# Kernel tuning notes

Measured on AMD Instinct MI355X. Metric: run time of the kernel, lower is better.

The kernel has to match this reference:

```python
import jax, jax.numpy as jnp
import numpy as np

N, D, L = 8192, 256, 3
DEGREE_P = 0.0078  # ~64 avg degree


def _normalize_adj(g):
    # symmetric normalization with self-loops: D^-1/2 (A + I) D^-1/2
    n = g.shape[0]
    a = g + jnp.eye(n, dtype=g.dtype)
    deg = jnp.sum(a, axis=1)
    dinv = jnp.where(deg > 0, jax.lax.rsqrt(deg), 0.0)
    return a * dinv[:, None] * dinv[None, :]


def _gcn(gn, h, W, b):
    # GCN layer (eval mode, dropout p=0): aggregate -> linear -> relu
    h = gn @ h                      # [N, D] adjacency aggregation
    return jax.nn.relu(h @ W.T + b)  # [N, D]


def setup_inputs() -> dict:
    key = jax.random.key(0)
    ks = jax.random.split(key, 8)
    # sparse binary symmetric adjacency stored dense
    g = (jax.random.uniform(ks[0], (N, N)) < DEGREE_P).astype(jnp.float32)
    g = jnp.maximum(g, g.T)
    h = jax.random.normal(ks[1], (N, D), dtype=jnp.float32)
    s = 1.0 / np.sqrt(D)
    W_down = jax.random.normal(ks[2], (L, D, D), dtype=jnp.float32) * s
    b_down = jnp.zeros((L, D), dtype=jnp.float32)
    W_bottom = jax.random.normal(ks[3], (D, D), dtype=jnp.float32) * s
    b_bottom = jnp.zeros((D,), dtype=jnp.float32)
    W_up = jax.random.normal(ks[4], (L, D, D), dtype=jnp.float32) * s
    b_up = jnp.zeros((L, D), dtype=jnp.float32)
    return dict(g=g, h=h, W_down=W_down, b_down=b_down,
                W_bottom=W_bottom, b_bottom=b_bottom,
                W_up=W_up, b_up=b_up)


def reference(g, h, W_down, b_down, W_bottom, b_bottom, W_up, b_up):
    gn = _normalize_adj(g)
    l_n = W_down.shape[0]
    org_h = h
    down_outs = []
    for i in range(l_n):
        h = _gcn(gn, h, W_down[i], b_down[i])
        down_outs.append(h)
    h = _gcn(gn, h, W_bottom, b_bottom)
    hs = []
    for i in range(l_n):
        h = h + down_outs[l_n - i - 1]   # skip connection
        h = _gcn(gn, h, W_up[i], b_up[i])
        hs.append(h)
    hs.append(h + org_h)
    return jnp.stack(hs)  # [l_n+1, N, D]
```

## Files before the change

### kernel.cpp

```cpp
#include <hip/hip_runtime.h>
#include <cstdint>
#include <cstddef>


#define GN 8192
#define GD 256
#define CAP 320

typedef unsigned int uint32;
using frag_ab = __attribute__((ext_vector_type(8))) short;
using frag_cd = __attribute__((ext_vector_type(4))) float;

static __device__ inline unsigned short f2bf(float x) {
    uint32 u = __float_as_uint(x);
    u += 0x7fffu + ((u >> 16) & 1u);
    return (unsigned short)(u >> 16);
}

__global__ __launch_bounds__(256) void k_build(const float* __restrict__ g,
                                               unsigned short* __restrict__ col,
                                               int* __restrict__ cnt,
                                               float* __restrict__ dinv)
{
    __shared__ int s_cnt;
    const int i = blockIdx.x;
    const int tid = threadIdx.x;
    if (tid == 0) s_cnt = 0;
    __syncthreads();
    const float4* grow = (const float4*)(g + (size_t)i * GN);
    unsigned short* crow = col + (size_t)i * CAP;
    for (int j4 = tid; j4 < GN / 4; j4 += 256) {
        float4 v = grow[j4];
        int j = j4 * 4;
        if (v.x != 0.0f) { int p = atomicAdd(&s_cnt, 1); if (p < CAP) crow[p] = (unsigned short)(j + 0); }
        if (v.y != 0.0f) { int p = atomicAdd(&s_cnt, 1); if (p < CAP) crow[p] = (unsigned short)(j + 1); }
        if (v.z != 0.0f) { int p = atomicAdd(&s_cnt, 1); if (p < CAP) crow[p] = (unsigned short)(j + 2); }
        if (v.w != 0.0f) { int p = atomicAdd(&s_cnt, 1); if (p < CAP) crow[p] = (unsigned short)(j + 3); }
    }
    __syncthreads();
    if (tid == 0) {
        int n = s_cnt; if (n > CAP) n = CAP;
        cnt[i] = n;
        dinv[i] = rsqrtf((float)s_cnt + 1.0f);
        int n8 = (n + 7) & ~7;
        for (int k = n; k < n8; ++k)
            if (k < CAP) crow[k] = (unsigned short)i;
    }
}

__global__ __launch_bounds__(256) void k_scale(const float* __restrict__ h,
                                               const float* __restrict__ dinv,
                                               unsigned short* __restrict__ hs_bf)
{
    int idx = blockIdx.x * 256 + threadIdx.x;
    float4 v = ((const float4*)h)[idx];
    int row = idx / (GD / 4);
    float dv = dinv[row];
    ushort4 r;
    r.x = f2bf(v.x * dv); r.y = f2bf(v.y * dv);
    r.z = f2bf(v.z * dv); r.w = f2bf(v.w * dv);
    ((ushort4*)hs_bf)[idx] = r;
}

__global__ __launch_bounds__(256) void k_f2bf(const float* __restrict__ src,
                                              unsigned short* __restrict__ dst)
{
    int idx = blockIdx.x * 256 + threadIdx.x;
    float4 v = ((const float4*)src)[idx];
    ushort4 r;
    r.x = f2bf(v.x); r.y = f2bf(v.y); r.z = f2bf(v.z); r.w = f2bf(v.w);
    ((ushort4*)dst)[idx] = r;
}

__global__ __launch_bounds__(256) void k_spmm(const uint32* __restrict__ hsw,
                                              const unsigned short* __restrict__ col,
                                              const int* __restrict__ cnt,
                                              const float* __restrict__ dinv,
                                              uint32* __restrict__ yw)
{
    const int tid  = threadIdx.x;
    const int lw   = tid >> 6;
    const int lane = tid & 63;
    const int i = blockIdx.x * 4 + lw;
    const int n = cnt[i];
    int n8 = (n + 7) & ~7; if (n8 > CAP) n8 = CAP;
    const uint4* idxp = (const uint4*)(col + (size_t)i * CAP);
    const uint32* lbase = hsw + lane * 2;

    float a0=0.f,a1=0.f,a2=0.f,a3=0.f;
    float b0=0.f,b1=0.f,b2=0.f,b3=0.f;

    for (int t8 = 0; t8 < n8; t8 += 8) {
        uint4 packed = idxp[t8 >> 3];
        uint32 p0 = (uint32)__builtin_amdgcn_readfirstlane((int)packed.x);
        uint32 p1 = (uint32)__builtin_amdgcn_readfirstlane((int)packed.y);
        uint32 p2 = (uint32)__builtin_amdgcn_readfirstlane((int)packed.z);
        uint32 p3 = (uint32)__builtin_amdgcn_readfirstlane((int)packed.w);
        const int c0 = (int)(p0 & 0xffffu), c1 = (int)(p0 >> 16);
        const int c2 = (int)(p1 & 0xffffu), c3 = (int)(p1 >> 16);
        const int c4 = (int)(p2 & 0xffffu), c5 = (int)(p2 >> 16);
        const int c6 = (int)(p3 & 0xffffu), c7 = (int)(p3 >> 16);
        uint2 u0 = *(const uint2*)(lbase + (size_t)c0 * 128);
        uint2 u1 = *(const uint2*)(lbase + (size_t)c1 * 128);
        uint2 u2 = *(const uint2*)(lbase + (size_t)c2 * 128);
        uint2 u3 = *(const uint2*)(lbase + (size_t)c3 * 128);
        uint2 u4 = *(const uint2*)(lbase + (size_t)c4 * 128);
        uint2 u5 = *(const uint2*)(lbase + (size_t)c5 * 128);
        uint2 u6 = *(const uint2*)(lbase + (size_t)c6 * 128);
        uint2 u7 = *(const uint2*)(lbase + (size_t)c7 * 128);
        a0 += __uint_as_float(u0.x << 16); a1 += __uint_as_float(u0.x & 0xffff0000u);
        a2 += __uint_as_float(u0.y << 16); a3 += __uint_as_float(u0.y & 0xffff0000u);
        b0 += __uint_as_float(u1.x << 16); b1 += __uint_as_float(u1.x & 0xffff0000u);
        b2 += __uint_as_float(u1.y << 16); b3 += __uint_as_float(u1.y & 0xffff0000u);
        a0 += __uint_as_float(u2.x << 16); a1 += __uint_as_float(u2.x & 0xffff0000u);
        a2 += __uint_as_float(u2.y << 16); a3 += __uint_as_float(u2.y & 0xffff0000u);
        b0 += __uint_as_float(u3.x << 16); b1 += __uint_as_float(u3.x & 0xffff0000u);
        b2 += __uint_as_float(u3.y << 16); b3 += __uint_as_float(u3.y & 0xffff0000u);
        a0 += __uint_as_float(u4.x << 16); a1 += __uint_as_float(u4.x & 0xffff0000u);
        a2 += __uint_as_float(u4.y << 16); a3 += __uint_as_float(u4.y & 0xffff0000u);
        b0 += __uint_as_float(u5.x << 16); b1 += __uint_as_float(u5.x & 0xffff0000u);
        b2 += __uint_as_float(u5.y << 16); b3 += __uint_as_float(u5.y & 0xffff0000u);
        a0 += __uint_as_float(u6.x << 16); a1 += __uint_as_float(u6.x & 0xffff0000u);
        a2 += __uint_as_float(u6.y << 16); a3 += __uint_as_float(u6.y & 0xffff0000u);
        b0 += __uint_as_float(u7.x << 16); b1 += __uint_as_float(u7.x & 0xffff0000u);
        b2 += __uint_as_float(u7.y << 16); b3 += __uint_as_float(u7.y & 0xffff0000u);
    }

    uint2 us = *(const uint2*)(lbase + (size_t)i * 128);
    const float coeff = (float)(1 - (n8 - n));
    a0 += coeff * __uint_as_float(us.x << 16);
    a1 += coeff * __uint_as_float(us.x & 0xffff0000u);
    a2 += coeff * __uint_as_float(us.y << 16);
    a3 += coeff * __uint_as_float(us.y & 0xffff0000u);

    const float dv = dinv[i];
    a0 = (a0 + b0) * dv; a1 = (a1 + b1) * dv;
    a2 = (a2 + b2) * dv; a3 = (a3 + b3) * dv;
    uint2 r;
    r.x = (uint32)f2bf(a0) | ((uint32)f2bf(a1) << 16);
    r.y = (uint32)f2bf(a2) | ((uint32)f2bf(a3) << 16);
    *(uint2*)(yw + (size_t)i * 128 + lane * 2) = r;
}

__global__ __launch_bounds__(256) void k_gemm(const unsigned short* __restrict__ Y,
                                              const unsigned short* __restrict__ W,
                                              const float* __restrict__ bias,
                                              const float* __restrict__ dinv,
                                              const float* __restrict__ skip,
                                              float* __restrict__ h_out,
                                              unsigned short* __restrict__ hs_out,
                                              float* __restrict__ sum_out,
                                              const float* __restrict__ add_src)
{
    const int tid  = threadIdx.x;
    const int w    = tid >> 6;
    const int lane = tid & 63;
    const int quad = lane >> 4;
    const int l16  = lane & 15;
    const int m0 = blockIdx.x * 64 + w * 16;
    const int n0 = blockIdx.y * 64;

    frag_cd acc0 = {0.f,0.f,0.f,0.f}, acc1 = {0.f,0.f,0.f,0.f};
    frag_cd acc2 = {0.f,0.f,0.f,0.f}, acc3 = {0.f,0.f,0.f,0.f};

    const size_t abase  = (size_t)(m0 + l16) * GD + quad * 8;
    const size_t bbase0 = (size_t)(n0 +  0 + l16) * GD + quad * 8;
    const size_t bbase1 = (size_t)(n0 + 16 + l16) * GD + quad * 8;
    const size_t bbase2 = (size_t)(n0 + 32 + l16) * GD + quad * 8;
    const size_t bbase3 = (size_t)(n0 + 48 + l16) * GD + quad * 8;

#pragma unroll
    for (int k0 = 0; k0 < GD; k0 += 32) {
        frag_ab a  = *(const frag_ab*)(Y + abase  + k0);
        frag_ab b0 = *(const frag_ab*)(W + bbase0 + k0);
        frag_ab b1 = *(const frag_ab*)(W + bbase1 + k0);
        frag_ab b2 = *(const frag_ab*)(W + bbase2 + k0);
        frag_ab b3 = *(const frag_ab*)(W + bbase3 + k0);
        acc0 = __builtin_amdgcn_mfma_f32_16x16x32_bf16(a, b0, acc0, 0, 0, 0);
        acc1 = __builtin_amdgcn_mfma_f32_16x16x32_bf16(a, b1, acc1, 0, 0, 0);
        acc2 = __builtin_amdgcn_mfma_f32_16x16x32_bf16(a, b2, acc2, 0, 0, 0);
        acc3 = __builtin_amdgcn_mfma_f32_16x16x32_bf16(a, b3, acc3, 0, 0, 0);
    }

    const float bn0 = bias[n0 +  0 + l16];
    const float bn1 = bias[n0 + 16 + l16];
    const float bn2 = bias[n0 + 32 + l16];
    const float bn3 = bias[n0 + 48 + l16];

#pragma unroll
    for (int reg = 0; reg < 4; ++reg) {
        const int m = m0 + quad * 4 + reg;
        const float dv = dinv[m];
        float v[4];
        v[0] = fmaxf(acc0[reg] + bn0, 0.f);
        v[1] = fmaxf(acc1[reg] + bn1, 0.f);
        v[2] = fmaxf(acc2[reg] + bn2, 0.f);
        v[3] = fmaxf(acc3[reg] + bn3, 0.f);
#pragma unroll
        for (int nt = 0; nt < 4; ++nt) {
            const size_t idx = (size_t)m * GD + n0 + nt * 16 + l16;
            const float x = v[nt];
            if (h_out)  h_out[idx] = x;
            if (hs_out) {
                float s = skip ? skip[idx] : 0.f;
                hs_out[idx] = f2bf(dv * (x + s));
            }
            if (sum_out) sum_out[idx] = x + add_src[idx];
        }
    }
}

extern "C" void kernel_launch(void* const* d_in, const int* in_sizes, int n_in,
                              void* d_out, int out_size, void* d_ws, size_t ws_size,
                              hipStream_t stream)
{
    const float* g  = (const float*)d_in[0];
    const float* h  = (const float*)d_in[1];
    const float* Wd = (const float*)d_in[2];
    const float* bd = (const float*)d_in[3];
    const float* Wb = (const float*)d_in[4];
    const float* bb = (const float*)d_in[5];
    const float* Wu = (const float*)d_in[6];
    const float* bu = (const float*)d_in[7];
    float* out = (float*)d_out;

    char* ws = (char*)d_ws;
    float*          dinv = (float*)ws;
    int*            cnt  = (int*)(ws + 32 * 1024);
    unsigned short* col  = (unsigned short*)(ws + 64 * 1024);
    size_t off = 64 * 1024 + (size_t)GN * CAP * sizeof(unsigned short);
    off = (off + 255) & ~(size_t)255;
    unsigned short* hs_bf = (unsigned short*)(ws + off); off += (size_t)GN * GD * 2;
    unsigned short* y_bf  = (unsigned short*)(ws + off); off += (size_t)GN * GD * 2;
    unsigned short* w_bf  = (unsigned short*)(ws + off); off += (size_t)7 * GD * GD * 2;
    off = (off + 255) & ~(size_t)255;
    float* dbuf1 = (float*)(ws + off); off += (size_t)GN * GD * 4;
    float* dbuf2 = (float*)(ws + off); off += (size_t)GN * GD * 4;
    float* dbuf3 = (float*)(ws + off); off += (size_t)GN * GD * 4;
    (void)ws_size; (void)in_sizes; (void)n_in; (void)out_size;

    const size_t ND = (size_t)GN * GD;
    const int WSZ = GD * GD;
    dim3 ggrid(GN / 64, GD / 64);
    dim3 sgrid(GN / 4);

    k_build<<<GN, 256, 0, stream>>>(g, col, cnt, dinv);
    k_scale<<<GN * GD / 4 / 256, 256, 0, stream>>>(h, dinv, hs_bf);
    k_f2bf<<<3 * WSZ / 4 / 256, 256, 0, stream>>>(Wd, w_bf + 0 * (size_t)WSZ);
    k_f2bf<<<1 * WSZ / 4 / 256, 256, 0, stream>>>(Wb, w_bf + 3 * (size_t)WSZ);
    k_f2bf<<<3 * WSZ / 4 / 256, 256, 0, stream>>>(Wu, w_bf + 4 * (size_t)WSZ);

    k_spmm<<<sgrid, 256, 0, stream>>>((const uint32*)hs_bf, col, cnt, dinv, (uint32*)y_bf);
    k_gemm<<<ggrid, 256, 0, stream>>>(y_bf, w_bf + 0 * (size_t)WSZ, bd + 0 * GD, dinv, nullptr, dbuf1, hs_bf, nullptr, nullptr);
    k_spmm<<<sgrid, 256, 0, stream>>>((const uint32*)hs_bf, col, cnt, dinv, (uint32*)y_bf);
    k_gemm<<<ggrid, 256, 0, stream>>>(y_bf, w_bf + 1 * (size_t)WSZ, bd + 1 * GD, dinv, nullptr, dbuf2, hs_bf, nullptr, nullptr);
    k_spmm<<<sgrid, 256, 0, stream>>>((const uint32*)hs_bf, col, cnt, dinv, (uint32*)y_bf);
    k_gemm<<<ggrid, 256, 0, stream>>>(y_bf, w_bf + 2 * (size_t)WSZ, bd + 2 * GD, dinv, nullptr, dbuf3, hs_bf, nullptr, nullptr);

    k_spmm<<<sgrid, 256, 0, stream>>>((const uint32*)hs_bf, col, cnt, dinv, (uint32*)y_bf);
    k_gemm<<<ggrid, 256, 0, stream>>>(y_bf, w_bf + 3 * (size_t)WSZ, bb, dinv, dbuf3, nullptr, hs_bf, nullptr, nullptr);

    k_spmm<<<sgrid, 256, 0, stream>>>((const uint32*)hs_bf, col, cnt, dinv, (uint32*)y_bf);
    k_gemm<<<ggrid, 256, 0, stream>>>(y_bf, w_bf + 4 * (size_t)WSZ, bu + 0 * GD, dinv, dbuf2, out + 0 * ND, hs_bf, nullptr, nullptr);
    k_spmm<<<sgrid, 256, 0, stream>>>((const uint32*)hs_bf, col, cnt, dinv, (uint32*)y_bf);
    k_gemm<<<ggrid, 256, 0, stream>>>(y_bf, w_bf + 5 * (size_t)WSZ, bu + 1 * GD, dinv, dbuf1, out + 1 * ND, hs_bf, nullptr, nullptr);
    k_spmm<<<sgrid, 256, 0, stream>>>((const uint32*)hs_bf, col, cnt, dinv, (uint32*)y_bf);
    k_gemm<<<ggrid, 256, 0, stream>>>(y_bf, w_bf + 6 * (size_t)WSZ, bu + 2 * GD, dinv, nullptr, out + 2 * ND, nullptr, out + 3 * ND, h);
}
```

Measured before the change: 785.3 us.

## Fuse SpMM aggregation and GEMM into one per-layer kernel with LDS staging

```diff
diff --git a/kernel.cpp b/kernel.cpp
--- a/kernel.cpp
+++ b/kernel.cpp
@@ -15,6 +15,9 @@
     uint32 u = __float_as_uint(x);
     u += 0x7fffu + ((u >> 16) & 1u);
     return (unsigned short)(u >> 16);
+}
+static __device__ inline uint32 pack2bf(float lo, float hi) {
+    return (uint32)f2bf(lo) | ((uint32)f2bf(hi) << 16);
 }
 
 __global__ __launch_bounds__(256) void k_build(const float* __restrict__ g,
@@ -42,9 +45,6 @@
         int n = s_cnt; if (n > CAP) n = CAP;
         cnt[i] = n;
         dinv[i] = rsqrtf((float)s_cnt + 1.0f);
-        int n8 = (n + 7) & ~7;
-        for (int k = n; k < n8; ++k)
-            if (k < CAP) crow[k] = (unsigned short)i;
     }
 }
 
@@ -72,98 +72,89 @@
     ((ushort4*)dst)[idx] = r;
 }
 
-__global__ __launch_bounds__(256) void k_spmm(const uint32* __restrict__ hsw,
-                                              const unsigned short* __restrict__ col,
-                                              const int* __restrict__ cnt,
-                                              const float* __restrict__ dinv,
-                                              uint32* __restrict__ yw)
-{
-    const int tid  = threadIdx.x;
-    const int lw   = tid >> 6;
-    const int lane = tid & 63;
-    const int i = blockIdx.x * 4 + lw;
-    const int n = cnt[i];
-    int n8 = (n + 7) & ~7; if (n8 > CAP) n8 = CAP;
-    const uint4* idxp = (const uint4*)(col + (size_t)i * CAP);
-    const uint32* lbase = hsw + lane * 2;
-
-    float a0=0.f,a1=0.f,a2=0.f,a3=0.f;
-    float b0=0.f,b1=0.f,b2=0.f,b3=0.f;
-
-    for (int t8 = 0; t8 < n8; t8 += 8) {
-        uint4 packed = idxp[t8 >> 3];
-        uint32 p0 = (uint32)__builtin_amdgcn_readfirstlane((int)packed.x);
-        uint32 p1 = (uint32)__builtin_amdgcn_readfirstlane((int)packed.y);
-        uint32 p2 = (uint32)__builtin_amdgcn_readfirstlane((int)packed.z);
-        uint32 p3 = (uint32)__builtin_amdgcn_readfirstlane((int)packed.w);
-        const int c0 = (int)(p0 & 0xffffu), c1 = (int)(p0 >> 16);
-        const int c2 = (int)(p1 & 0xffffu), c3 = (int)(p1 >> 16);
-        const int c4 = (int)(p2 & 0xffffu), c5 = (int)(p2 >> 16);
-        const int c6 = (int)(p3 & 0xffffu), c7 = (int)(p3 >> 16);
-        uint2 u0 = *(const uint2*)(lbase + (size_t)c0 * 128);
-        uint2 u1 = *(const uint2*)(lbase + (size_t)c1 * 128);
-        uint2 u2 = *(const uint2*)(lbase + (size_t)c2 * 128);
-        uint2 u3 = *(const uint2*)(lbase + (size_t)c3 * 128);
-        uint2 u4 = *(const uint2*)(lbase + (size_t)c4 * 128);
-        uint2 u5 = *(const uint2*)(lbase + (size_t)c5 * 128);
-        uint2 u6 = *(const uint2*)(lbase + (size_t)c6 * 128);
-        uint2 u7 = *(const uint2*)(lbase + (size_t)c7 * 128);
-        a0 += __uint_as_float(u0.x << 16); a1 += __uint_as_float(u0.x & 0xffff0000u);
-        a2 += __uint_as_float(u0.y << 16); a3 += __uint_as_float(u0.y & 0xffff0000u);
-        b0 += __uint_as_float(u1.x << 16); b1 += __uint_as_float(u1.x & 0xffff0000u);
-        b2 += __uint_as_float(u1.y << 16); b3 += __uint_as_float(u1.y & 0xffff0000u);
-        a0 += __uint_as_float(u2.x << 16); a1 += __uint_as_float(u2.x & 0xffff0000u);
-        a2 += __uint_as_float(u2.y << 16); a3 += __uint_as_float(u2.y & 0xffff0000u);
-        b0 += __uint_as_float(u3.x << 16); b1 += __uint_as_float(u3.x & 0xffff0000u);
-        b2 += __uint_as_float(u3.y << 16); b3 += __uint_as_float(u3.y & 0xffff0000u);
-        a0 += __uint_as_float(u4.x << 16); a1 += __uint_as_float(u4.x & 0xffff0000u);
-        a2 += __uint_as_float(u4.y << 16); a3 += __uint_as_float(u4.y & 0xffff0000u);
-        b0 += __uint_as_float(u5.x << 16); b1 += __uint_as_float(u5.x & 0xffff0000u);
-        b2 += __uint_as_float(u5.y << 16); b3 += __uint_as_float(u5.y & 0xffff0000u);
-        a0 += __uint_as_float(u6.x << 16); a1 += __uint_as_float(u6.x & 0xffff0000u);
-        a2 += __uint_as_float(u6.y << 16); a3 += __uint_as_float(u6.y & 0xffff0000u);
-        b0 += __uint_as_float(u7.x << 16); b1 += __uint_as_float(u7.x & 0xffff0000u);
-        b2 += __uint_as_float(u7.y << 16); b3 += __uint_as_float(u7.y & 0xffff0000u);
-    }
-
-    uint2 us = *(const uint2*)(lbase + (size_t)i * 128);
-    const float coeff = (float)(1 - (n8 - n));
-    a0 += coeff * __uint_as_float(us.x << 16);
-    a1 += coeff * __uint_as_float(us.x & 0xffff0000u);
-    a2 += coeff * __uint_as_float(us.y << 16);
-    a3 += coeff * __uint_as_float(us.y & 0xffff0000u);
-
-    const float dv = dinv[i];
-    a0 = (a0 + b0) * dv; a1 = (a1 + b1) * dv;
-    a2 = (a2 + b2) * dv; a3 = (a3 + b3) * dv;
-    uint2 r;
-    r.x = (uint32)f2bf(a0) | ((uint32)f2bf(a1) << 16);
-    r.y = (uint32)f2bf(a2) | ((uint32)f2bf(a3) << 16);
-    *(uint2*)(yw + (size_t)i * 128 + lane * 2) = r;
-}
-
-__global__ __launch_bounds__(256) void k_gemm(const unsigned short* __restrict__ Y,
-                                              const unsigned short* __restrict__ W,
-                                              const float* __restrict__ bias,
-                                              const float* __restrict__ dinv,
-                                              const float* __restrict__ skip,
-                                              float* __restrict__ h_out,
-                                              unsigned short* __restrict__ hs_out,
-                                              float* __restrict__ sum_out,
-                                              const float* __restrict__ add_src)
-{
+__global__ __launch_bounds__(256) void k_layer(const uint32* __restrict__ hs_in,
+                                               const unsigned short* __restrict__ col,
+                                               const int* __restrict__ cnt,
+                                               const float* __restrict__ dinv,
+                                               const unsigned short* __restrict__ W,
+                                               const float* __restrict__ bias,
+                                               const float* __restrict__ skip,
+                                               float* __restrict__ h_out,
+                                               unsigned short* __restrict__ hs_out,
+                                               float* __restrict__ sum_out,
+                                               const float* __restrict__ add_src)
+{
+    __shared__ unsigned short s_idx[16][CAP];
+    __shared__ unsigned short s_y[16][264];
     const int tid  = threadIdx.x;
     const int w    = tid >> 6;
     const int lane = tid & 63;
+    const int m0   = blockIdx.x * 16;
+
+    const uint32* lbase = hs_in + lane * 2;
+#pragma unroll 1
+    for (int rr = 0; rr < 4; ++rr) {
+        const int lrow = w * 4 + rr;
+        const int i = m0 + lrow;
+        const int n = cnt[i];
+        unsigned short* si = s_idx[lrow];
+        for (int t = lane; t < n; t += 64) si[t] = col[(size_t)i * CAP + t];
+
+        float a0=0.f,a1=0.f,a2=0.f,a3=0.f;
+        float b0=0.f,b1=0.f,b2=0.f,b3=0.f;
+        int t = 0;
+        for (; t + 8 <= n; t += 8) {
+            int c0=si[t],c1=si[t+1],c2=si[t+2],c3=si[t+3];
+            int c4=si[t+4],c5=si[t+5],c6=si[t+6],c7=si[t+7];
+            uint2 u0 = *(const uint2*)(lbase + (size_t)c0 * 128);
+            uint2 u1 = *(const uint2*)(lbase + (size_t)c1 * 128);
+            uint2 u2 = *(const uint2*)(lbase + (size_t)c2 * 128);
+            uint2 u3 = *(const uint2*)(lbase + (size_t)c3 * 128);
+            uint2 u4 = *(const uint2*)(lbase + (size_t)c4 * 128);
+            uint2 u5 = *(const uint2*)(lbase + (size_t)c5 * 128);
+            uint2 u6 = *(const uint2*)(lbase + (size_t)c6 * 128);
+            uint2 u7 = *(const uint2*)(lbase + (size_t)c7 * 128);
+            a0 += __uint_as_float(u0.x << 16); a1 += __uint_as_float(u0.x & 0xffff0000u);
+            a2 += __uint_as_float(u0.y << 16); a3 += __uint_as_float(u0.y & 0xffff0000u);
+            b0 += __uint_as_float(u1.x << 16); b1 += __uint_as_float(u1.x & 0xffff0000u);
+            b2 += __uint_as_float(u1.y << 16); b3 += __uint_as_float(u1.y & 0xffff0000u);
+            a0 += __uint_as_float(u2.x << 16); a1 += __uint_as_float(u2.x & 0xffff0000u);
+            a2 += __uint_as_float(u2.y << 16); a3 += __uint_as_float(u2.y & 0xffff0000u);
+            b0 += __uint_as_float(u3.x << 16); b1 += __uint_as_float(u3.x & 0xffff0000u);
+            b2 += __uint_as_float(u3.y << 16); b3 += __uint_as_float(u3.y & 0xffff0000u);
+            a0 += __uint_as_float(u4.x << 16); a1 += __uint_as_float(u4.x & 0xffff0000u);
+            a2 += __uint_as_float(u4.y << 16); a3 += __uint_as_float(u4.y & 0xffff0000u);
+            b0 += __uint_as_float(u5.x << 16); b1 += __uint_as_float(u5.x & 0xffff0000u);
+            b2 += __uint_as_float(u5.y << 16); b3 += __uint_as_float(u5.y & 0xffff0000u);
+            a0 += __uint_as_float(u6.x << 16); a1 += __uint_as_float(u6.x & 0xffff0000u);
+            a2 += __uint_as_float(u6.y << 16); a3 += __uint_as_float(u6.y & 0xffff0000u);
+            b0 += __uint_as_float(u7.x << 16); b1 += __uint_as_float(u7.x & 0xffff0000u);
+            b2 += __uint_as_float(u7.y << 16); b3 += __uint_as_float(u7.y & 0xffff0000u);
+        }
+        for (; t < n; ++t) {
+            uint2 u = *(const uint2*)(lbase + (size_t)si[t] * 128);
+            a0 += __uint_as_float(u.x << 16); a1 += __uint_as_float(u.x & 0xffff0000u);
+            a2 += __uint_as_float(u.y << 16); a3 += __uint_as_float(u.y & 0xffff0000u);
+        }
+        uint2 us = *(const uint2*)(lbase + (size_t)i * 128);
+        a0 += __uint_as_float(us.x << 16); a1 += __uint_as_float(us.x & 0xffff0000u);
+        a2 += __uint_as_float(us.y << 16); a3 += __uint_as_float(us.y & 0xffff0000u);
+        const float dv = dinv[i];
+        a0 = (a0 + b0) * dv; a1 = (a1 + b1) * dv;
+        a2 = (a2 + b2) * dv; a3 = (a3 + b3) * dv;
+        uint32* yrow = (uint32*)s_y[lrow];
+        yrow[lane * 2 + 0] = pack2bf(a0, a1);
+        yrow[lane * 2 + 1] = pack2bf(a2, a3);
+    }
+    __syncthreads();
+
     const int quad = lane >> 4;
     const int l16  = lane & 15;
-    const int m0 = blockIdx.x * 64 + w * 16;
-    const int n0 = blockIdx.y * 64;
+    const int n0   = w * 64;
 
     frag_cd acc0 = {0.f,0.f,0.f,0.f}, acc1 = {0.f,0.f,0.f,0.f};
     frag_cd acc2 = {0.f,0.f,0.f,0.f}, acc3 = {0.f,0.f,0.f,0.f};
 
-    const size_t abase  = (size_t)(m0 + l16) * GD + quad * 8;
     const size_t bbase0 = (size_t)(n0 +  0 + l16) * GD + quad * 8;
     const size_t bbase1 = (size_t)(n0 + 16 + l16) * GD + quad * 8;
     const size_t bbase2 = (size_t)(n0 + 32 + l16) * GD + quad * 8;
@@ -171,7 +162,7 @@
 
 #pragma unroll
     for (int k0 = 0; k0 < GD; k0 += 32) {
-        frag_ab a  = *(const frag_ab*)(Y + abase  + k0);
+        frag_ab a  = *(const frag_ab*)&s_y[l16][quad * 8 + k0];
         frag_ab b0 = *(const frag_ab*)(W + bbase0 + k0);
         frag_ab b1 = *(const frag_ab*)(W + bbase1 + k0);
         frag_ab b2 = *(const frag_ab*)(W + bbase2 + k0);
@@ -230,9 +221,9 @@
     unsigned short* col  = (unsigned short*)(ws + 64 * 1024);
     size_t off = 64 * 1024 + (size_t)GN * CAP * sizeof(unsigned short);
     off = (off + 255) & ~(size_t)255;
-    unsigned short* hs_bf = (unsigned short*)(ws + off); off += (size_t)GN * GD * 2;
-    unsigned short* y_bf  = (unsigned short*)(ws + off); off += (size_t)GN * GD * 2;
-    unsigned short* w_bf  = (unsigned short*)(ws + off); off += (size_t)7 * GD * GD * 2;
+    unsigned short* hs_a = (unsigned short*)(ws + off); off += (size_t)GN * GD * 2;
+    unsigned short* hs_b = (unsigned short*)(ws + off); off += (size_t)GN * GD * 2;
+    unsigned short* w_bf = (unsigned short*)(ws + off); off += (size_t)7 * GD * GD * 2;
     off = (off + 255) & ~(size_t)255;
     float* dbuf1 = (float*)(ws + off); off += (size_t)GN * GD * 4;
     float* dbuf2 = (float*)(ws + off); off += (size_t)GN * GD * 4;
@@ -241,29 +232,26 @@
 
     const size_t ND = (size_t)GN * GD;
     const int WSZ = GD * GD;
-    dim3 ggrid(GN / 64, GD / 64);
-    dim3 sgrid(GN / 4);
+    dim3 lgrid(GN / 16);
 
     k_build<<<GN, 256, 0, stream>>>(g, col, cnt, dinv);
-    k_scale<<<GN * GD / 4 / 256, 256, 0, stream>>>(h, dinv, hs_bf);
+    k_scale<<<GN * GD / 4 / 256, 256, 0, stream>>>(h, dinv, hs_a);
     k_f2bf<<<3 * WSZ / 4 / 256, 256, 0, stream>>>(Wd, w_bf + 0 * (size_t)WSZ);
     k_f2bf<<<1 * WSZ / 4 / 256, 256, 0, stream>>>(Wb, w_bf + 3 * (size_t)WSZ);
     k_f2bf<<<3 * WSZ / 4 / 256, 256, 0, stream>>>(Wu, w_bf + 4 * (size_t)WSZ);
 
-    k_spmm<<<sgrid, 256, 0, stream>>>((const uint32*)hs_bf, col, cnt, dinv, (uint32*)y_bf);
-    k_gemm<<<ggrid, 256, 0, stream>>>(y_bf, w_bf + 0 * (size_t)WSZ, bd + 0 * GD, dinv, nullptr, dbuf1, hs_bf, nullptr, nullptr);
-    k_spmm<<<sgrid, 256, 0, stream>>>((const uint32*)hs_bf, col, cnt, dinv, (uint32*)y_bf);
-    k_gemm<<<ggrid, 256, 0, stream>>>(y_bf, w_bf + 1 * (size_t)WSZ, bd + 1 * GD, dinv, nullptr, dbuf2, hs_bf, nullptr, nullptr);
-    k_spmm<<<sgrid, 256, 0, stream>>>((const uint32*)hs_bf, col, cnt, dinv, (uint32*)y_bf);
-    k_gemm<<<ggrid, 256, 0, stream>>>(y_bf, w_bf + 2 * (size_t)WSZ, bd + 2 * GD, dinv, nullptr, dbuf3, hs_bf, nullptr, nullptr);
-
-    k_spmm<<<sgrid, 256, 0, stream>>>((const uint32*)hs_bf, col, cnt, dinv, (uint32*)y_bf);
-    k_gemm<<<ggrid, 256, 0, stream>>>(y_bf, w_bf + 3 * (size_t)WSZ, bb, dinv, dbuf3, nullptr, hs_bf, nullptr, nullptr);
-
-    k_spmm<<<sgrid, 256, 0, stream>>>((const uint32*)hs_bf, col, cnt, dinv, (uint32*)y_bf);
-    k_gemm<<<ggrid, 256, 0, stream>>>(y_bf, w_bf + 4 * (size_t)WSZ, bu + 0 * GD, dinv, dbuf2, out + 0 * ND, hs_bf, nullptr, nullptr);
-    k_spmm<<<sgrid, 256, 0, stream>>>((const uint32*)hs_bf, col, cnt, dinv, (uint32*)y_bf);
-    k_gemm<<<ggrid, 256, 0, stream>>>(y_bf, w_bf + 5 * (size_t)WSZ, bu + 1 * GD, dinv, dbuf1, out + 1 * ND, hs_bf, nullptr, nullptr);
-    k_spmm<<<sgrid, 256, 0, stream>>>((const uint32*)hs_bf, col, cnt, dinv, (uint32*)y_bf);
-    k_gemm<<<ggrid, 256, 0, stream>>>(y_bf, w_bf + 6 * (size_t)WSZ, bu + 2 * GD, dinv, nullptr, out + 2 * ND, nullptr, out + 3 * ND, h);
-}
+    k_layer<<<lgrid, 256, 0, stream>>>((const uint32*)hs_a, col, cnt, dinv,
+        w_bf + 0 * (size_t)WSZ, bd + 0 * GD, nullptr, dbuf1, hs_b, nullptr, nullptr);
+    k_layer<<<lgrid, 256, 0, stream>>>((const uint32*)hs_b, col, cnt, dinv,
+        w_bf + 1 * (size_t)WSZ, bd + 1 * GD, nullptr, dbuf2, hs_a, nullptr, nullptr);
+    k_layer<<<lgrid, 256, 0, stream>>>((const uint32*)hs_a, col, cnt, dinv,
+        w_bf + 2 * (size_t)WSZ, bd + 2 * GD, nullptr, dbuf3, hs_b, nullptr, nullptr);
+    k_layer<<<lgrid, 256, 0, stream>>>((const uint32*)hs_b, col, cnt, dinv,
+        w_bf + 3 * (size_t)WSZ, bb, dbuf3, nullptr, hs_a, nullptr, nullptr);
+    k_layer<<<lgrid, 256, 0, stream>>>((const uint32*)hs_a, col, cnt, dinv,
+        w_bf + 4 * (size_t)WSZ, bu + 0 * GD, dbuf2, out + 0 * ND, hs_b, nullptr, nullptr);
+    k_layer<<<lgrid, 256, 0, stream>>>((const uint32*)hs_b, col, cnt, dinv,
+        w_bf + 5 * (size_t)WSZ, bu + 1 * GD, dbuf1, out + 1 * ND, hs_a, nullptr, nullptr);
+    k_layer<<<lgrid, 256, 0, stream>>>((const uint32*)hs_a, col, cnt, dinv,
+        w_bf + 6 * (size_t)WSZ, bu + 2 * GD, nullptr, out + 2 * ND, nullptr, out + 3 * ND, h);
+}
```

Measured after the change: 768.5 us. -2.1%, faster.
